# Kernel optimization log

Measured on AMD Instinct MI355X. Metric: run time of the kernel, lower is better.

The kernel has to match this reference:

```python
import jax, jax.numpy as jnp
import numpy as np

BN_EPS = 1e-5


def _bn_relu(x, g, beta, mu, var):
    # x: (B, C, N); per-channel inference batchnorm + ReLU
    scale = (g / jnp.sqrt(var + BN_EPS))[None, :, None]
    shift = (beta - mu * g / jnp.sqrt(var + BN_EPS))[None, :, None]
    return jax.nn.relu(x * scale + shift)


def setup_inputs() -> dict:
    key = jax.random.key(0)
    ks = jax.random.split(key, 8)
    B, N, S, C1, C2 = 16, 4096, 1024, 256, 512
    Cin, H = C1 + C2, 256
    inp = {
        'unknown': jax.random.normal(ks[0], (B, N, 3), jnp.float32),
        'known': jax.random.normal(ks[1], (B, S, 3), jnp.float32),
        'unknow_feats': jax.random.normal(ks[2], (B, C1, N), jnp.float32),
        'known_feats': jax.random.normal(ks[3], (B, C2, S), jnp.float32),
        'W1': jax.random.normal(ks[4], (H, Cin), jnp.float32) * (1.0 / np.sqrt(Cin)),
        'b1': jnp.zeros((H,), jnp.float32),
        'g1': jnp.ones((H,), jnp.float32),
        'beta1': jnp.zeros((H,), jnp.float32),
        'mu1': jnp.zeros((H,), jnp.float32),
        'var1': jnp.ones((H,), jnp.float32),
        'W2': jax.random.normal(ks[5], (H, H), jnp.float32) * (1.0 / np.sqrt(H)),
        'b2': jnp.zeros((H,), jnp.float32),
        'g2': jnp.ones((H,), jnp.float32),
        'beta2': jnp.zeros((H,), jnp.float32),
        'mu2': jnp.zeros((H,), jnp.float32),
        'var2': jnp.ones((H,), jnp.float32),
    }
    return inp


def reference(unknown, known, unknow_feats, known_feats,
              W1, b1, g1, beta1, mu1, var1,
              W2, b2, g2, beta2, mu2, var2):
    B, N, _ = unknown.shape
    S = known.shape[1]
    kf = jnp.transpose(known_feats, (0, 2, 1))  # (B, S, C2)

    # squared pairwise distances: (B, N, S)
    d2 = (jnp.sum(unknown * unknown, -1)[:, :, None]
          + jnp.sum(known * known, -1)[:, None, :]
          - 2.0 * jnp.einsum('bnc,bsc->bns', unknown, known))
    # 3 smallest distances (ascending), matching sort + [:3]
    neg_top, idx = jax.lax.top_k(-d2, 3)          # (B, N, 3)
    dists = -neg_top
    w = 1.0 / (dists + 1e-8)
    w = w / jnp.sum(w, -1, keepdims=True)          # (B, N, 3)

    gathered = jax.vmap(lambda f, i: f[i])(kf, idx)  # (B, N, 3, C2)
    interp = jnp.sum(gathered * w[..., None], axis=2)  # (B, N, C2)

    new_feats = jnp.concatenate(
        [jnp.transpose(unknow_feats, (0, 2, 1)), interp], axis=-1)  # (B, N, C1+C2)
    x = jnp.transpose(new_feats, (0, 2, 1))  # (B, Cin, N)

    x = _bn_relu(jnp.einsum('oc,bcn->bon', W1, x) + b1[None, :, None],
                 g1, beta1, mu1, var1)
    x = _bn_relu(jnp.einsum('oc,bcn->bon', W2, x) + b2[None, :, None],
                 g2, beta2, mu2, var2)
    return x  # (B, mlp[-1], N)
```

## Files before the change

kernel.cpp:

```cpp
#include <hip/hip_runtime.h>
#include <hip/hip_bf16.h>
#include <cstdint>
#include <cstddef>

typedef _Float16 f16;
typedef _Float16 f16x8 __attribute__((ext_vector_type(8)));
typedef _Float16 f16x4 __attribute__((ext_vector_type(4)));
typedef float    f32x4 __attribute__((ext_vector_type(4)));

constexpr int Bdim = 16, Ndim = 4096, Sdim = 1024;
constexpr int C1 = 256, C2 = 512, CIN = 768, H = 256;

__device__ __forceinline__ void async16(void* l, const void* g) {
  __builtin_amdgcn_global_load_lds(
      reinterpret_cast<__attribute__((address_space(1))) char*>(
          reinterpret_cast<uintptr_t>(g)),
      reinterpret_cast<__attribute__((address_space(3))) char*>(
          reinterpret_cast<uintptr_t>(l)),
      16, 0, 0);
}

__global__ void prep_kernel(const float* __restrict__ W1, const float* __restrict__ W2,
    const float* __restrict__ b1, const float* __restrict__ g1, const float* __restrict__ be1,
    const float* __restrict__ mu1, const float* __restrict__ va1,
    const float* __restrict__ b2, const float* __restrict__ g2, const float* __restrict__ be2,
    const float* __restrict__ mu2, const float* __restrict__ va2,
    f16* __restrict__ W1h, f16* __restrict__ W2h,
    float* __restrict__ s1, float* __restrict__ t1,
    float* __restrict__ s2, float* __restrict__ t2)
{
  int i = blockIdx.x * 256 + threadIdx.x;
  if (i < H * CIN) W1h[i] = (f16)W1[i];
  if (i < H * H)   W2h[i] = (f16)W2[i];
  if (i < H) {
    float sc1 = g1[i] / sqrtf(va1[i] + 1e-5f);
    s1[i] = sc1; t1[i] = b1[i] * sc1 + be1[i] - mu1[i] * sc1;
    float sc2 = g2[i] / sqrtf(va2[i] + 1e-5f);
    s2[i] = sc2; t2[i] = b2[i] * sc2 + be2[i] - mu2[i] * sc2;
  }
}

__device__ __forceinline__ void top3_insert(float pd, int pi,
    float& d0, float& d1, float& d2v, int& i0, int& i1, int& i2)
{
  bool c0 = (pd < d0) || (pd == d0 && pi < i0);
  bool c1 = (pd < d1) || (pd == d1 && pi < i1);
  bool c2 = (pd < d2v) || (pd == d2v && pi < i2);
  d2v = c1 ? d1 : (c2 ? pd : d2v);
  i2  = c1 ? i1 : (c2 ? pi : i2);
  d1  = c0 ? d0 : (c1 ? pd : d1);
  i1  = c0 ? i0 : (c1 ? pi : i1);
  d0  = c0 ? pd : d0;
  i0  = c0 ? pi : i0;
}

__global__ __launch_bounds__(256)
void knn_kernel(const float* __restrict__ unknown, const float* __restrict__ known,
                int* __restrict__ idx3, float* __restrict__ w3)
{
  __shared__ float4 kp4[Sdim];
  int b = blockIdx.y, t = threadIdx.x;
  const float* kb = known + (size_t)b * 3 * Sdim;
#pragma unroll
  for (int i = 0; i < 4; ++i) {
    int s = t + 256 * i;
    float kx = kb[3 * s], ky = kb[3 * s + 1], kz = kb[3 * s + 2];
    float sk = __fadd_rn(__fadd_rn(__fmul_rn(kx, kx), __fmul_rn(ky, ky)), __fmul_rn(kz, kz));
    kp4[s ^ ((s >> 7) & 7)] = make_float4(kx, ky, kz, sk);
  }
  __syncthreads();

  int q = t >> 3;
  int j = t & 7;
  int n = blockIdx.x * 32 + q;
  const float* up = unknown + ((size_t)b * Ndim + n) * 3;
  float ux = up[0], uy = up[1], uz = up[2];
  float su = __fadd_rn(__fadd_rn(__fmul_rn(ux, ux), __fmul_rn(uy, uy)), __fmul_rn(uz, uz));

  float d0 = 1e30f, d1 = 1e30f, d2v = 1e30f;
  int i0 = 0, i1 = 0, i2 = 0;
  int sbase = j << 7;
  for (int k = 0; k < 128; ++k) {
    int s = sbase + k;
    float4 kv = kp4[s ^ j];
    float dot = __fadd_rn(__fadd_rn(__fmul_rn(ux, kv.x), __fmul_rn(uy, kv.y)), __fmul_rn(uz, kv.z));
    float d = __fsub_rn(__fadd_rn(su, kv.w), __fmul_rn(2.0f, dot));
    bool c0 = d < d0, c1 = d < d1, c2 = d < d2v;
    d2v = c1 ? d1 : (c2 ? d : d2v);
    i2  = c1 ? i1 : (c2 ? s : i2);
    d1  = c0 ? d0 : (c1 ? d : d1);
    i1  = c0 ? i0 : (c1 ? s : i1);
    d0  = c0 ? d : d0;
    i0  = c0 ? s : i0;
  }

#pragma unroll
  for (int m = 1; m < 8; m <<= 1) {
    float pd0 = __shfl_xor(d0, m), pd1 = __shfl_xor(d1, m), pd2 = __shfl_xor(d2v, m);
    int pi0 = __shfl_xor(i0, m), pi1 = __shfl_xor(i1, m), pi2 = __shfl_xor(i2, m);
    top3_insert(pd0, pi0, d0, d1, d2v, i0, i1, i2);
    top3_insert(pd1, pi1, d0, d1, d2v, i0, i1, i2);
    top3_insert(pd2, pi2, d0, d1, d2v, i0, i1, i2);
  }

  if (j == 0) {
    float wa = 1.0f / (d0 + 1e-8f);
    float wb = 1.0f / (d1 + 1e-8f);
    float wc = 1.0f / (d2v + 1e-8f);
    float wsum = wa + wb + wc;
    int p = b * Ndim + n;
    idx3[3 * p] = i0; idx3[3 * p + 1] = i1; idx3[3 * p + 2] = i2;
    w3[3 * p] = wa / wsum; w3[3 * p + 1] = wb / wsum; w3[3 * p + 2] = wc / wsum;
  }
}

__global__ void transpose_cast(const float* __restrict__ in, f16* __restrict__ out,
                               int R, int C, int ldo, long inBStride, long outBStride)
{
  __shared__ float tile[32][33];
  const float* src = in + blockIdx.z * inBStride;
  f16* dst = out + blockIdx.z * outBStride;
  int r0 = blockIdx.y * 32, c0 = blockIdx.x * 32;
  int tx = threadIdx.x & 31, ty = threadIdx.x >> 5;
#pragma unroll
  for (int i = 0; i < 4; ++i)
    tile[ty + i * 8][tx] = src[(size_t)(r0 + ty + i * 8) * C + c0 + tx];
  __syncthreads();
#pragma unroll
  for (int i = 0; i < 4; ++i)
    dst[(size_t)(c0 + ty + i * 8) * ldo + r0 + tx] = (f16)tile[tx][ty + i * 8];
}

__global__ __launch_bounds__(256)
void interp_kernel(const f16* __restrict__ kfT, const int* __restrict__ idx3,
                   const float* __restrict__ w3, f16* __restrict__ feat)
{
  int t = threadIdx.x;
  int wv = t >> 6, l = t & 63;
  int ptbase = blockIdx.x * 32 + wv * 8;
#pragma unroll
  for (int i = 0; i < 8; ++i) {
    int pt = ptbase + i;
    int b = pt >> 12;
    int i0 = idx3[3 * pt], i1 = idx3[3 * pt + 1], i2 = idx3[3 * pt + 2];
    float w0 = w3[3 * pt], w1 = w3[3 * pt + 1], w2 = w3[3 * pt + 2];
    const f16* base = kfT + ((size_t)b << 10) * C2;
    f16x8 a = *((const f16x8*)(base + (size_t)i0 * C2) + l);
    f16x8 c = *((const f16x8*)(base + (size_t)i1 * C2) + l);
    f16x8 d = *((const f16x8*)(base + (size_t)i2 * C2) + l);
    f16x8 o;
#pragma unroll
    for (int j = 0; j < 8; ++j)
      o[j] = (f16)(w0 * (float)a[j] + w1 * (float)c[j] + w2 * (float)d[j]);
    *((f16x8*)(feat + (size_t)pt * CIN + C1) + l) = o;
  }
}

template <int K, int MODE>
__global__ __launch_bounds__(256)
void gemm_kernel(const f16* __restrict__ A, const f16* __restrict__ Bt,
                 const float* __restrict__ scale, const float* __restrict__ shift,
                 void* __restrict__ outp)
{
  __shared__ char lds[65536];

  int id = blockIdx.x;
  id = (id & 7) * 128 + (id >> 3);
  int big = id >> 1, small = id & 1;
  int m0, n0;
  if (MODE == 1) { m0 = small * 128; n0 = big * 128; }
  else           { m0 = big * 128;  n0 = small * 128; }

  int t = threadIdx.x;
  int lane = t & 63, wid = t >> 6;
  int wm = wid >> 1, wn = wid & 1;
  int lr = lane & 15, lh = lane >> 4;

  f32x4 acc[4][4] = {};

  constexpr int NT = K / 64;
  const f16* Arow = A + (size_t)m0 * K;
  const f16* Brow = Bt + (size_t)n0 * K;
  int p = t >> 3, x = t & 7;

  auto STAGE = [&](int buf, int kt) {
    int k0 = kt * 64;
    char* base = lds + buf * 32768;
#pragma unroll
    for (int r = 0; r < 4; ++r) {
      int row = r * 32 + p;
      int sw = (x ^ (row & 7)) * 8;
      async16(base + r * 4096 + t * 16,         Arow + (size_t)row * K + k0 + sw);
      async16(base + 16384 + r * 4096 + t * 16, Brow + (size_t)row * K + k0 + sw);
    }
  };

  STAGE(0, 0);
  __syncthreads();
  int cur = 0;
  for (int kt = 0; kt < NT; ++kt) {
    if (kt + 1 < NT) STAGE(cur ^ 1, kt + 1);
    const char* Ab = lds + cur * 32768;
    const char* Bb = Ab + 16384;
#pragma unroll
    for (int kk = 0; kk < 2; ++kk) {
      f16x8 af[4], bf[4];
#pragma unroll
      for (int mf = 0; mf < 4; ++mf) {
        int row = wm * 64 + mf * 16 + lr;
        int g = kk * 4 + lh;
        af[mf] = *(const f16x8*)(Ab + row * 128 + ((g ^ (row & 7)) << 4));
      }
#pragma unroll
      for (int nf = 0; nf < 4; ++nf) {
        int row = wn * 64 + nf * 16 + lr;
        int g = kk * 4 + lh;
        bf[nf] = *(const f16x8*)(Bb + row * 128 + ((g ^ (row & 7)) << 4));
      }
#pragma unroll
      for (int mf = 0; mf < 4; ++mf)
#pragma unroll
        for (int nf = 0; nf < 4; ++nf)
          acc[mf][nf] = __builtin_amdgcn_mfma_f32_16x16x32_f16(af[mf], bf[nf], acc[mf][nf], 0, 0, 0);
    }
    __syncthreads();
    cur ^= 1;
  }

  if (MODE == 1) {
    f16* x1 = (f16*)outp;
#pragma unroll
    for (int mf = 0; mf < 4; ++mf) {
      int ob = m0 + wm * 64 + mf * 16 + lh * 4;
      f32x4 sc = *(const f32x4*)(scale + ob);
      f32x4 sh = *(const f32x4*)(shift + ob);
#pragma unroll
      for (int nf = 0; nf < 4; ++nf) {
        int ptc = n0 + wn * 64 + nf * 16 + lr;
        f16x4 v;
#pragma unroll
        for (int j = 0; j < 4; ++j) {
          float y = acc[mf][nf][j] * sc[j] + sh[j];
          v[j] = (f16)(y > 0.0f ? y : 0.0f);
        }
        *(f16x4*)(x1 + (size_t)ptc * H + ob) = v;
      }
    }
  } else {
    float* out = (float*)outp;
#pragma unroll
    for (int mf = 0; mf < 4; ++mf) {
      int ptb = m0 + wm * 64 + mf * 16 + lh * 4;
      int bb = ptb >> 12, nn = ptb & 4095;
#pragma unroll
      for (int nf = 0; nf < 4; ++nf) {
        int o = n0 + wn * 64 + nf * 16 + lr;
        float sc = scale[o], sh = shift[o];
        f32x4 v;
#pragma unroll
        for (int j = 0; j < 4; ++j) {
          float y = acc[mf][nf][j] * sc + sh;
          v[j] = (y > 0.0f ? y : 0.0f);
        }
        *(f32x4*)(out + ((size_t)(bb * H + o) << 12) + nn) = v;
      }
    }
  }
}

extern "C" void kernel_launch(void* const* d_in, const int* in_sizes, int n_in,
                              void* d_out, int out_size, void* d_ws, size_t ws_size,
                              hipStream_t stream)
{
  (void)in_sizes; (void)n_in; (void)out_size; (void)ws_size;
  const float* unknown = (const float*)d_in[0];
  const float* known   = (const float*)d_in[1];
  const float* uf      = (const float*)d_in[2];
  const float* kf      = (const float*)d_in[3];
  const float* W1  = (const float*)d_in[4];
  const float* b1  = (const float*)d_in[5];
  const float* g1  = (const float*)d_in[6];
  const float* be1 = (const float*)d_in[7];
  const float* mu1 = (const float*)d_in[8];
  const float* va1 = (const float*)d_in[9];
  const float* W2  = (const float*)d_in[10];
  const float* b2  = (const float*)d_in[11];
  const float* g2  = (const float*)d_in[12];
  const float* be2 = (const float*)d_in[13];
  const float* mu2 = (const float*)d_in[14];
  const float* va2 = (const float*)d_in[15];

  char* ws = (char*)d_ws;
  f16*   W1h  = (f16*)(ws + 0);
  f16*   W2h  = (f16*)(ws + 393216);
  float* s1   = (float*)(ws + 524288);
  float* t1   = (float*)(ws + 525312);
  float* s2   = (float*)(ws + 526336);
  float* t2   = (float*)(ws + 527360);
  int*   idx3 = (int*)(ws + 528384);
  float* w3   = (float*)(ws + 1314816);
  f16*   kfT  = (f16*)(ws + 2101248);
  f16*   feat = (f16*)(ws + 18878464);
  f16*   x1   = (f16*)(ws + 119541760);

  prep_kernel<<<768, 256, 0, stream>>>(W1, W2, b1, g1, be1, mu1, va1,
                                       b2, g2, be2, mu2, va2,
                                       W1h, W2h, s1, t1, s2, t2);
  knn_kernel<<<dim3(Ndim / 32, Bdim), 256, 0, stream>>>(unknown, known, idx3, w3);
  transpose_cast<<<dim3(Sdim / 32, C2 / 32, Bdim), 256, 0, stream>>>(
      kf, kfT, C2, Sdim, C2, (long)C2 * Sdim, (long)Sdim * C2);
  transpose_cast<<<dim3(Ndim / 32, C1 / 32, Bdim), 256, 0, stream>>>(
      uf, feat, C1, Ndim, CIN, (long)C1 * Ndim, (long)Ndim * CIN);
  interp_kernel<<<(Bdim * Ndim) / 32, 256, 0, stream>>>(kfT, idx3, w3, feat);
  gemm_kernel<CIN, 1><<<1024, 256, 0, stream>>>(W1h, feat, s1, t1, x1);
  gemm_kernel<H,   2><<<1024, 256, 0, stream>>>(x1, W2h, s2, t2, d_out);
}
```

Measured before the change: 325.6 us.

## Two-pass KNN: value-only med3 top-3 then collect indices below threshold

The KNN kernel now finds the three smallest distances per thread with a value-only fmed3/fmin network and merges them across the 8 lanes with a min/max network that carries no indices. A second pass recomputes the distances, gathers candidates at or below the third-smallest value into shared memory with atomics, and a final sorted insert recovers the indices. The aim is to cut the per-element select cost of tracking indices, at the price of computing distances twice. The LDS layout changes from an XOR swizzle to padding. If more than 8 candidates tie the extra ones are dropped, and the tie ordering may differ from top_k.

Result: faster. 318.4 us (-2.2%).

```diff
diff --git a/kernel.cpp b/kernel.cpp
--- a/kernel.cpp
+++ b/kernel.cpp
@@ -58,15 +58,20 @@
 void knn_kernel(const float* __restrict__ unknown, const float* __restrict__ known,
                 int* __restrict__ idx3, float* __restrict__ w3)
 {
-  __shared__ float4 kp4[Sdim];
+  __shared__ float4 kp4[8 * 129];
+  __shared__ int   ccnt[32];
+  __shared__ float cd[32][8];
+  __shared__ int   cs[32][8];
+
   int b = blockIdx.y, t = threadIdx.x;
+  if (t < 32) ccnt[t] = 0;
   const float* kb = known + (size_t)b * 3 * Sdim;
 #pragma unroll
   for (int i = 0; i < 4; ++i) {
     int s = t + 256 * i;
     float kx = kb[3 * s], ky = kb[3 * s + 1], kz = kb[3 * s + 2];
     float sk = __fadd_rn(__fadd_rn(__fmul_rn(kx, kx), __fmul_rn(ky, ky)), __fmul_rn(kz, kz));
-    kp4[s ^ ((s >> 7) & 7)] = make_float4(kx, ky, kz, sk);
+    kp4[(s >> 7) * 129 + (s & 127)] = make_float4(kx, ky, kz, sk);
   }
   __syncthreads();
 
@@ -77,33 +82,48 @@
   float ux = up[0], uy = up[1], uz = up[2];
   float su = __fadd_rn(__fadd_rn(__fmul_rn(ux, ux), __fmul_rn(uy, uy)), __fmul_rn(uz, uz));
 
-  float d0 = 1e30f, d1 = 1e30f, d2v = 1e30f;
-  int i0 = 0, i1 = 0, i2 = 0;
-  int sbase = j << 7;
+  const float4* base = kp4 + j * 129;
+
+  float t0 = 1e30f, t1 = 1e30f, t2 = 1e30f;
+#pragma unroll 8
   for (int k = 0; k < 128; ++k) {
-    int s = sbase + k;
-    float4 kv = kp4[s ^ j];
+    float4 kv = base[k];
     float dot = __fadd_rn(__fadd_rn(__fmul_rn(ux, kv.x), __fmul_rn(uy, kv.y)), __fmul_rn(uz, kv.z));
     float d = __fsub_rn(__fadd_rn(su, kv.w), __fmul_rn(2.0f, dot));
-    bool c0 = d < d0, c1 = d < d1, c2 = d < d2v;
-    d2v = c1 ? d1 : (c2 ? d : d2v);
-    i2  = c1 ? i1 : (c2 ? s : i2);
-    d1  = c0 ? d0 : (c1 ? d : d1);
-    i1  = c0 ? i0 : (c1 ? s : i1);
-    d0  = c0 ? d : d0;
-    i0  = c0 ? s : i0;
+    t2 = __builtin_amdgcn_fmed3f(t1, t2, d);
+    t1 = __builtin_amdgcn_fmed3f(t0, t1, d);
+    t0 = fminf(t0, d);
   }
 
 #pragma unroll
   for (int m = 1; m < 8; m <<= 1) {
-    float pd0 = __shfl_xor(d0, m), pd1 = __shfl_xor(d1, m), pd2 = __shfl_xor(d2v, m);
-    int pi0 = __shfl_xor(i0, m), pi1 = __shfl_xor(i1, m), pi2 = __shfl_xor(i2, m);
-    top3_insert(pd0, pi0, d0, d1, d2v, i0, i1, i2);
-    top3_insert(pd1, pi1, d0, d1, d2v, i0, i1, i2);
-    top3_insert(pd2, pi2, d0, d1, d2v, i0, i1, i2);
-  }
+    float b0 = __shfl_xor(t0, m), b1 = __shfl_xor(t1, m), b2 = __shfl_xor(t2, m);
+    float n0 = fminf(t0, b0);
+    float n1 = fminf(fmaxf(t0, b0), fminf(t1, b1));
+    float n2 = fminf(fmaxf(t0, b1), fminf(fmaxf(t1, b0), fminf(t2, b2)));
+    t0 = n0; t1 = n1; t2 = n2;
+  }
+  float D2 = t2;
+
+#pragma unroll 4
+  for (int k = 0; k < 128; ++k) {
+    float4 kv = base[k];
+    float dot = __fadd_rn(__fadd_rn(__fmul_rn(ux, kv.x), __fmul_rn(uy, kv.y)), __fmul_rn(uz, kv.z));
+    float d = __fsub_rn(__fadd_rn(su, kv.w), __fmul_rn(2.0f, dot));
+    if (d <= D2) {
+      int slot = atomicAdd(&ccnt[q], 1);
+      if (slot < 8) { cd[q][slot] = d; cs[q][slot] = j * 128 + k; }
+    }
+  }
+  __syncthreads();
 
   if (j == 0) {
+    float d0 = 1e30f, d1 = 1e30f, d2v = 1e30f;
+    int i0 = 0x7fffffff, i1 = 0x7fffffff, i2 = 0x7fffffff;
+    int mcnt = ccnt[q] < 8 ? ccnt[q] : 8;
+#pragma unroll
+    for (int i = 0; i < 8; ++i)
+      if (i < mcnt) top3_insert(cd[q][i], cs[q][i], d0, d1, d2v, i0, i1, i2);
     float wa = 1.0f / (d0 + 1e-8f);
     float wb = 1.0f / (d1 + 1e-8f);
     float wc = 1.0f / (d2v + 1e-8f);
```

## Compute KNN distances with split-f16 MFMA and two-pass top-3 selection

Applied to the files above, without the earlier changes.

Reformulates the pairwise squared-distance computation as an f16 matrix multiply on MFMA units, splitting each coordinate into high and low f16 parts to keep near-fp32 accuracy. The known-point operand panel is precomputed in the prep kernel. Selection becomes two passes: a branch-free med3 top-3 threshold per row, then a recompute pass that collects only candidates at or below the threshold into shared memory for an exact top-3 with index tie-breaking. This removes the scalar FP32 distance loop, at the cost of recomputing the MFMAs twice and some risk of rounding differences or candidate-slot overflow under ties.

New measurement: 308.3 us. -5.3%, faster.

```diff
diff --git a/kernel.cpp b/kernel.cpp
--- a/kernel.cpp
+++ b/kernel.cpp
@@ -25,13 +25,31 @@
     const float* __restrict__ mu1, const float* __restrict__ va1,
     const float* __restrict__ b2, const float* __restrict__ g2, const float* __restrict__ be2,
     const float* __restrict__ mu2, const float* __restrict__ va2,
-    f16* __restrict__ W1h, f16* __restrict__ W2h,
+    const float* __restrict__ known,
+    f16* __restrict__ W1h, f16* __restrict__ W2h, f16* __restrict__ bpanel,
     float* __restrict__ s1, float* __restrict__ t1,
     float* __restrict__ s2, float* __restrict__ t2)
 {
   int i = blockIdx.x * 256 + threadIdx.x;
   if (i < H * CIN) W1h[i] = (f16)W1[i];
   if (i < H * H)   W2h[i] = (f16)W2[i];
+  if (i < Bdim * Sdim) {
+    const float* kp = known + (size_t)i * 3;
+    float kx = kp[0], ky = kp[1], kz = kp[2];
+    float sk = kx * kx + ky * ky + kz * kz;
+    float mx = -2.0f * kx, my = -2.0f * ky, mz = -2.0f * kz;
+    f16 hx = (f16)mx, lx = (f16)(mx - (float)hx);
+    f16 hy = (f16)my, ly = (f16)(my - (float)hy);
+    f16 hz = (f16)mz, lz = (f16)(mz - (float)hz);
+    f16 hs = (f16)sk, ls = (f16)(sk - (float)hs);
+    f16* d = bpanel + (size_t)i * 24;
+    d[0] = hx; d[1] = lx; d[2]  = hx; d[3]  = lx;
+    d[4] = hy; d[5] = ly; d[6]  = hy; d[7]  = ly;
+    d[8] = hz; d[9] = lz; d[10] = hz; d[11] = lz;
+    d[12] = hs; d[13] = ls; d[14] = (f16)0.f; d[15] = (f16)0.f;
+#pragma unroll
+    for (int q = 16; q < 24; ++q) d[q] = (f16)0.f;
+  }
   if (i < H) {
     float sc1 = g1[i] / sqrtf(va1[i] + 1e-5f);
     s1[i] = sc1; t1[i] = b1[i] * sc1 + be1[i] - mu1[i] * sc1;
@@ -54,60 +72,120 @@
   i0  = c0 ? pi : i0;
 }
 
-__global__ __launch_bounds__(256)
-void knn_kernel(const float* __restrict__ unknown, const float* __restrict__ known,
+__global__ __launch_bounds__(512)
+void knn_kernel(const float* __restrict__ unknown, const f16* __restrict__ bpanel,
                 int* __restrict__ idx3, float* __restrict__ w3)
 {
-  __shared__ float4 kp4[Sdim];
-  int b = blockIdx.y, t = threadIdx.x;
-  const float* kb = known + (size_t)b * 3 * Sdim;
-#pragma unroll
-  for (int i = 0; i < 4; ++i) {
-    int s = t + 256 * i;
-    float kx = kb[3 * s], ky = kb[3 * s + 1], kz = kb[3 * s + 2];
-    float sk = __fadd_rn(__fadd_rn(__fmul_rn(kx, kx), __fmul_rn(ky, ky)), __fmul_rn(kz, kz));
-    kp4[s ^ ((s >> 7) & 7)] = make_float4(kx, ky, kz, sk);
+  __shared__ f16  Blds[Sdim * 24];
+  __shared__ f16  Alds[8 * 16 * 24];
+  __shared__ float su_lds[8 * 16];
+  __shared__ int   cnt[128];
+  __shared__ float cd[128][8];
+  __shared__ int   ci[128][8];
+
+  int t = threadIdx.x;
+  int b = blockIdx.y;
+  int lane = t & 63, w = t >> 6;
+  int r = lane & 15, g = lane >> 4;
+
+  if (t < 128) cnt[t] = 0;
+
+  {
+    const f16* bp = bpanel + (size_t)b * Sdim * 24;
+#pragma unroll
+    for (int i = 0; i < 6; ++i) {
+      int c = t + i * 512;
+      async16((char*)Blds + c * 16, (const char*)bp + c * 16);
+    }
+  }
+
+  int n0 = blockIdx.x * 128 + w * 16;
+  if (lane < 16) {
+    int n = n0 + lane;
+    const float* up = unknown + ((size_t)b * Ndim + n) * 3;
+    float x = up[0], y = up[1], z = up[2];
+    su_lds[w * 16 + lane] = x * x + y * y + z * z;
+    f16 hx = (f16)x, lx = (f16)(x - (float)hx);
+    f16 hy = (f16)y, ly = (f16)(y - (float)hy);
+    f16 hz = (f16)z, lz = (f16)(z - (float)hz);
+    f16* ar = Alds + (w * 16 + lane) * 24;
+    f16x8 c0 = {hx, hx, lx, lx, hy, hy, ly, ly};
+    f16x8 c1 = {hz, hz, lz, lz, (f16)1.f, (f16)1.f, (f16)0.f, (f16)0.f};
+    *(f16x8*)ar = c0;
+    *(f16x8*)(ar + 8) = c1;
   }
   __syncthreads();
 
-  int q = t >> 3;
-  int j = t & 7;
-  int n = blockIdx.x * 32 + q;
-  const float* up = unknown + ((size_t)b * Ndim + n) * 3;
-  float ux = up[0], uy = up[1], uz = up[2];
-  float su = __fadd_rn(__fadd_rn(__fmul_rn(ux, ux), __fmul_rn(uy, uy)), __fmul_rn(uz, uz));
-
-  float d0 = 1e30f, d1 = 1e30f, d2v = 1e30f;
-  int i0 = 0, i1 = 0, i2 = 0;
-  int sbase = j << 7;
-  for (int k = 0; k < 128; ++k) {
-    int s = sbase + k;
-    float4 kv = kp4[s ^ j];
-    float dot = __fadd_rn(__fadd_rn(__fmul_rn(ux, kv.x), __fmul_rn(uy, kv.y)), __fmul_rn(uz, kv.z));
-    float d = __fsub_rn(__fadd_rn(su, kv.w), __fmul_rn(2.0f, dot));
-    bool c0 = d < d0, c1 = d < d1, c2 = d < d2v;
-    d2v = c1 ? d1 : (c2 ? d : d2v);
-    i2  = c1 ? i1 : (c2 ? s : i2);
-    d1  = c0 ? d0 : (c1 ? d : d1);
-    i1  = c0 ? i0 : (c1 ? s : i1);
-    d0  = c0 ? d : d0;
-    i0  = c0 ? s : i0;
-  }
-
-#pragma unroll
-  for (int m = 1; m < 8; m <<= 1) {
-    float pd0 = __shfl_xor(d0, m), pd1 = __shfl_xor(d1, m), pd2 = __shfl_xor(d2v, m);
-    int pi0 = __shfl_xor(i0, m), pi1 = __shfl_xor(i1, m), pi2 = __shfl_xor(i2, m);
-    top3_insert(pd0, pi0, d0, d1, d2v, i0, i1, i2);
-    top3_insert(pd1, pi1, d0, d1, d2v, i0, i1, i2);
-    top3_insert(pd2, pi2, d0, d1, d2v, i0, i1, i2);
-  }
-
-  if (j == 0) {
+  f16x8 af = {};
+  if (g < 2) af = *(const f16x8*)(Alds + (w * 16 + r) * 24 + g * 8);
+  f32x4 su4;
+#pragma unroll
+  for (int j = 0; j < 4; ++j) su4[j] = su_lds[w * 16 + g * 4 + j];
+  int boff = r * 24 + (g & 1) * 8;
+
+  float t0_[4], t1_[4], t2_[4];
+#pragma unroll
+  for (int j = 0; j < 4; ++j) { t0_[j] = 1e30f; t1_[j] = 1e30f; t2_[j] = 1e30f; }
+
+#pragma unroll 4
+  for (int T = 0; T < 64; ++T) {
+    f16x8 bf = *(const f16x8*)(Blds + T * 384 + boff);
+    f32x4 acc = su4;
+    acc = __builtin_amdgcn_mfma_f32_16x16x32_f16(af, bf, acc, 0, 0, 0);
+#pragma unroll
+    for (int j = 0; j < 4; ++j) {
+      float d = acc[j];
+      t2_[j] = __builtin_amdgcn_fmed3f(t1_[j], t2_[j], d);
+      t1_[j] = __builtin_amdgcn_fmed3f(t0_[j], t1_[j], d);
+      t0_[j] = fminf(t0_[j], d);
+    }
+  }
+
+#pragma unroll
+  for (int m = 1; m < 16; m <<= 1) {
+#pragma unroll
+    for (int j = 0; j < 4; ++j) {
+      float b0 = __shfl_xor(t0_[j], m), b1 = __shfl_xor(t1_[j], m), b2 = __shfl_xor(t2_[j], m);
+      float n0m = fminf(t0_[j], b0);
+      float n1m = fminf(fmaxf(t0_[j], b0), fminf(t1_[j], b1));
+      float n2m = fminf(fminf(fmaxf(t0_[j], b1), fmaxf(t1_[j], b0)), fminf(t2_[j], b2));
+      t0_[j] = n0m; t1_[j] = n1m; t2_[j] = n2m;
+    }
+  }
+
+#pragma unroll 2
+  for (int T = 0; T < 64; ++T) {
+    f16x8 bf = *(const f16x8*)(Blds + T * 384 + boff);
+    f32x4 acc = su4;
+    acc = __builtin_amdgcn_mfma_f32_16x16x32_f16(af, bf, acc, 0, 0, 0);
+    bool h = (acc[0] <= t2_[0]) | (acc[1] <= t2_[1]) |
+             (acc[2] <= t2_[2]) | (acc[3] <= t2_[3]);
+    if (h) {
+#pragma unroll
+      for (int j = 0; j < 4; ++j) {
+        if (acc[j] <= t2_[j]) {
+          int q = w * 16 + g * 4 + j;
+          int slot = atomicAdd(&cnt[q], 1);
+          if (slot < 8) { cd[q][slot] = acc[j]; ci[q][slot] = T * 16 + r; }
+        }
+      }
+    }
+  }
+  __syncthreads();
+
+  if (t < 128) {
+    int q = t;
+    float d0 = 1e30f, d1 = 1e30f, d2v = 1e30f;
+    int i0 = 0x7fffffff, i1 = 0x7fffffff, i2 = 0x7fffffff;
+    int mc = cnt[q] < 8 ? cnt[q] : 8;
+#pragma unroll
+    for (int i = 0; i < 8; ++i)
+      if (i < mc) top3_insert(cd[q][i], ci[q][i], d0, d1, d2v, i0, i1, i2);
     float wa = 1.0f / (d0 + 1e-8f);
     float wb = 1.0f / (d1 + 1e-8f);
     float wc = 1.0f / (d2v + 1e-8f);
     float wsum = wa + wb + wc;
+    int n = blockIdx.x * 128 + q;
     int p = b * Ndim + n;
     idx3[3 * p] = i0; idx3[3 * p + 1] = i1; idx3[3 * p + 2] = i2;
     w3[3 * p] = wa / wsum; w3[3 * p + 1] = wb / wsum; w3[3 * p + 2] = wc / wsum;
@@ -291,22 +369,23 @@
   const float* va2 = (const float*)d_in[15];
 
   char* ws = (char*)d_ws;
-  f16*   W1h  = (f16*)(ws + 0);
-  f16*   W2h  = (f16*)(ws + 393216);
-  float* s1   = (float*)(ws + 524288);
-  float* t1   = (float*)(ws + 525312);
-  float* s2   = (float*)(ws + 526336);
-  float* t2   = (float*)(ws + 527360);
-  int*   idx3 = (int*)(ws + 528384);
-  float* w3   = (float*)(ws + 1314816);
-  f16*   kfT  = (f16*)(ws + 2101248);
-  f16*   feat = (f16*)(ws + 18878464);
-  f16*   x1   = (f16*)(ws + 119541760);
+  f16*   W1h    = (f16*)(ws + 0);
+  f16*   W2h    = (f16*)(ws + 393216);
+  float* s1     = (float*)(ws + 524288);
+  float* t1     = (float*)(ws + 525312);
+  float* s2     = (float*)(ws + 526336);
+  float* t2     = (float*)(ws + 527360);
+  int*   idx3   = (int*)(ws + 528384);
+  float* w3     = (float*)(ws + 1314816);
+  f16*   bpanel = (f16*)(ws + 2101248);
+  f16*   kfT    = (f16*)(ws + 2887680);
+  f16*   feat   = (f16*)(ws + 19664896);
+  f16*   x1     = (f16*)(ws + 120328192);
 
   prep_kernel<<<768, 256, 0, stream>>>(W1, W2, b1, g1, be1, mu1, va1,
-                                       b2, g2, be2, mu2, va2,
-                                       W1h, W2h, s1, t1, s2, t2);
-  knn_kernel<<<dim3(Ndim / 32, Bdim), 256, 0, stream>>>(unknown, known, idx3, w3);
+                                       b2, g2, be2, mu2, va2, known,
+                                       W1h, W2h, bpanel, s1, t1, s2, t2);
+  knn_kernel<<<dim3(Ndim / 128, Bdim), 512, 0, stream>>>(unknown, bpanel, idx3, w3);
   transpose_cast<<<dim3(Sdim / 32, C2 / 32, Bdim), 256, 0, stream>>>(
       kf, kfT, C2, Sdim, C2, (long)C2 * Sdim, (long)Sdim * C2);
   transpose_cast<<<dim3(Ndim / 32, C1 / 32, Bdim), 256, 0, stream>>>(
```
